# Optimization experiments

Hardware: AMD Instinct MI355X
Metric: run time of the kernel (lower is better)

## Reference

```python
import jax, jax.numpy as jnp
import numpy as np
import math

ALPHA = 2.0   # ATan surrogate default alpha
TAU = 2.0     # LIF tau
VTH = 1.0     # v_threshold default
EPS = 1e-5    # BatchNorm eps
T, N, C, H, W = 16, 32, 128, 32, 32
COUT = 128

@jax.custom_vjp
def atan_spike(x):
    return (x >= 0).astype(x.dtype)

def _spike_fwd(x):
    return (x >= 0).astype(x.dtype), x

def _spike_bwd(x, g):
    return (g * (ALPHA / 2) / (1.0 + (math.pi / 2 * ALPHA * x) ** 2),)

atan_spike.defvjp(_spike_fwd, _spike_bwd)

def lif_scan(x):
    # MultiStepLIFNode, decay_input=False, v_reset=0.0, detach_reset=True:
    #   v <- v + (x_t - (v - 0)) / tau ; spike = H(v - vth) ; v <- v * (1 - sg(spike))
    def step(v, x_t):
        v = v + (x_t - v) / TAU
        s = atan_spike(v - VTH)
        v = v * (1.0 - jax.lax.stop_gradient(s))
        return v, s
    v0 = jnp.zeros_like(x[0])
    _, spikes = jax.lax.scan(step, v0, x)
    return spikes  # [T, N, C, H, W]

def setup_inputs() -> dict:
    key = jax.random.key(0)
    ks = jax.random.split(key, 9)
    x = jax.random.normal(ks[0], (T, N, C, H, W), dtype=jnp.float32)
    dw_w = jax.random.normal(ks[1], (C, 1, 3, 3), dtype=jnp.float32) * (1.0 / 3.0)
    dw_b = jax.random.normal(ks[2], (C,), dtype=jnp.float32) * 0.01
    pw_w = jax.random.normal(ks[3], (COUT, C), dtype=jnp.float32) * (1.0 / math.sqrt(C))
    pw_b = jax.random.normal(ks[4], (COUT,), dtype=jnp.float32) * 0.01
    gamma = jnp.ones((COUT,), dtype=jnp.float32)
    beta = jnp.zeros((COUT,), dtype=jnp.float32)
    run_mean = jax.random.normal(ks[5], (COUT,), dtype=jnp.float32) * 0.1
    run_var = jax.random.uniform(ks[6], (COUT,), dtype=jnp.float32) + 0.5
    return {"x": x, "dw_w": dw_w, "dw_b": dw_b, "pw_w": pw_w, "pw_b": pw_b,
            "gamma": gamma, "beta": beta, "run_mean": run_mean, "run_var": run_var}

def reference(x, dw_w, dw_b, pw_w, pw_b, gamma, beta, run_mean, run_var):
    s = lif_scan(x)                          # [T,N,C,H,W] spikes
    s2 = s.reshape(T * N, C, H, W)           # seq_to_ann_forward flattening
    # depthwise 3x3, stride 1, pad 1
    y = jax.lax.conv_general_dilated(
        s2, dw_w, window_strides=(1, 1), padding="SAME",
        feature_group_count=C,
        dimension_numbers=("NCHW", "OIHW", "NCHW"))
    y = y + dw_b[None, :, None, None]
    # pointwise 1x1
    y = jnp.einsum("nchw,oc->nohw", y, pw_w) + pw_b[None, :, None, None]
    # BatchNorm2d (inference mode, running stats)
    scale = gamma / jnp.sqrt(run_var + EPS)
    y = (y - run_mean[None, :, None, None]) * scale[None, :, None, None] + beta[None, :, None, None]
    return y.reshape(T, N, COUT, H, W)
```

## Files before the change

### kernel.cpp

```cpp
#include <hip/hip_runtime.h>
#include <hip/hip_bf16.h>
#include <stdint.h>

#define T_    16
#define N_    32
#define C_    128
#define HW_   1024
#define COUT_ 128

typedef __bf16 bf16x8 __attribute__((ext_vector_type(8)));
typedef float  f32x4  __attribute__((ext_vector_type(4)));

__global__ __launch_bounds__(256) void k0_prep(
    const float* __restrict__ pw_w, const float* __restrict__ pw_b,
    const float* __restrict__ gamma, const float* __restrict__ beta,
    const float* __restrict__ mean,  const float* __restrict__ var,
    __bf16* __restrict__ wbf, float* __restrict__ scale2, float* __restrict__ bias2) {
  int idx = blockIdx.x * 256 + threadIdx.x;
  if (idx < COUT_ * C_) wbf[idx] = (__bf16)pw_w[idx];
  if (idx < COUT_) {
    float s = gamma[idx] * rsqrtf(var[idx] + 1e-5f);
    scale2[idx] = s;
    bias2[idx]  = beta[idx] + (pw_b[idx] - mean[idx]) * s;
  }
}

__global__ __launch_bounds__(256) void k1_lif(const float* __restrict__ x,
                                              uint32_t* __restrict__ S) {
  int nc   = blockIdx.x;
  int tid  = threadIdx.x;
  int lane = tid & 63;
  int w    = tid >> 6;
  size_t base = (size_t)nc * HW_;
  unsigned long long* S64 = (unsigned long long*)S;

  float v0 = 0.f, v1 = 0.f, v2 = 0.f, v3 = 0.f;
#pragma unroll
  for (int t = 0; t < T_; ++t) {
    const float* xp = x + (size_t)t * (N_ * C_ * HW_) + base;
    float x0 = xp[tid];
    float x1 = xp[256 + tid];
    float x2 = xp[512 + tid];
    float x3 = xp[768 + tid];
    v0 = v0 + (x0 - v0) * 0.5f; bool s0 = (v0 >= 1.0f); if (s0) v0 = 0.f;
    v1 = v1 + (x1 - v1) * 0.5f; bool s1 = (v1 >= 1.0f); if (s1) v1 = 0.f;
    v2 = v2 + (x2 - v2) * 0.5f; bool s2 = (v2 >= 1.0f); if (s2) v2 = 0.f;
    v3 = v3 + (x3 - v3) * 0.5f; bool s3 = (v3 >= 1.0f); if (s3) v3 = 0.f;
    unsigned long long m0 = __ballot(s0);
    unsigned long long m1 = __ballot(s1);
    unsigned long long m2 = __ballot(s2);
    unsigned long long m3 = __ballot(s3);
    if (lane == 0) {
      size_t b64 = ((size_t)nc * T_ + t) * 16;
      S64[b64 + 0  + w] = m0;
      S64[b64 + 4  + w] = m1;
      S64[b64 + 8  + w] = m2;
      S64[b64 + 12 + w] = m3;
    }
  }
}

__global__ __launch_bounds__(256) void k2_main(
    const uint32_t* __restrict__ S,
    const float* __restrict__ dww, const float* __restrict__ dwb,
    const __bf16* __restrict__ wbf,
    const float* __restrict__ scale2, const float* __restrict__ bias2,
    float* __restrict__ out) {
  __shared__ uint32_t sb[C_ * 8];
  __shared__ __bf16  Blds[128 * 136];

  const int bid   = blockIdx.x;
  const int n_img = bid >> 3;
  const int rg    = bid & 7;
  const int t_img = n_img >> 5;
  const int n_in  = n_img & 31;
  const int r0    = rg * 4;
  const int tid   = threadIdx.x;

#pragma unroll
  for (int k = 0; k < 3; ++k) {
    int li = k * 256 + tid;
    int c  = li / 6;
    int ri = li - c * 6;
    int gr = r0 - 1 + ri;
    uint32_t wv = 0;
    if (gr >= 0 && gr < 32)
      wv = S[(((size_t)n_in * C_ + c) * T_ + t_img) * 32 + gr];
    sb[c * 8 + ri] = wv;
  }
  __syncthreads();

  {
    int c    = tid & 127;
    int half = tid >> 7;
    float w9[9];
#pragma unroll
    for (int i = 0; i < 9; ++i) w9[i] = dww[c * 9 + i];
    float bias = dwb[c];
    uint64_t R[6];
#pragma unroll
    for (int q = 0; q < 6; ++q) R[q] = ((uint64_t)sb[c * 8 + q]) << 1;

    int col0 = half * 16;
#pragma unroll 4
    for (int ci = 0; ci < 16; ++ci) {
      int col = col0 + ci;
      float acc[4] = {bias, bias, bias, bias};
#pragma unroll
      for (int q = 0; q < 6; ++q) {
        uint32_t tri = (uint32_t)(R[q] >> col) & 7u;
        float b0 = (float)(tri & 1u);
        float b1 = (float)((tri >> 1) & 1u);
        float b2 = (float)(tri >> 2);
#pragma unroll
        for (int kh = 0; kh < 3; ++kh) {
          int r = q - kh;
          if (r >= 0 && r < 4) {
            acc[r] += w9[kh * 3 + 0] * b0;
            acc[r] += w9[kh * 3 + 1] * b1;
            acc[r] += w9[kh * 3 + 2] * b2;
          }
        }
      }
#pragma unroll
      for (int r = 0; r < 4; ++r)
        Blds[(r * 32 + col) * 136 + c] = (__bf16)acc[r];
    }
  }
  __syncthreads();

  const int lane  = tid & 63;
  const int wid   = tid >> 6;
  const int ohalf = wid >> 1;
  const int hhalf = wid & 1;
  const int m16   = lane & 15;
  const int q4    = lane >> 4;

  f32x4 acc[4][4];
#pragma unroll
  for (int mt = 0; mt < 4; ++mt)
#pragma unroll
    for (int nt = 0; nt < 4; ++nt)
      acc[mt][nt] = (f32x4){0.f, 0.f, 0.f, 0.f};

#pragma unroll
  for (int ks = 0; ks < 4; ++ks) {
    const int k0 = ks * 32 + q4 * 8;
    bf16x8 af[4], bfr[4];
#pragma unroll
    for (int mt = 0; mt < 4; ++mt) {
      int m = ohalf * 64 + mt * 16 + m16;
      af[mt] = *(const bf16x8*)(wbf + m * 128 + k0);
    }
#pragma unroll
    for (int nt = 0; nt < 4; ++nt) {
      int hw = hhalf * 64 + nt * 16 + m16;
      bfr[nt] = *(const bf16x8*)(Blds + hw * 136 + k0);
    }
#pragma unroll
    for (int nt = 0; nt < 4; ++nt)
#pragma unroll
      for (int mt = 0; mt < 4; ++mt)
        acc[mt][nt] = __builtin_amdgcn_mfma_f32_16x16x32_bf16(af[mt], bfr[nt], acc[mt][nt], 0, 0, 0);
  }

#pragma unroll
  for (int mt = 0; mt < 4; ++mt) {
    int ob = ohalf * 64 + mt * 16 + q4 * 4;
    f32x4 sc = *(const f32x4*)(scale2 + ob);
    f32x4 bs = *(const f32x4*)(bias2 + ob);
#pragma unroll
    for (int nt = 0; nt < 4; ++nt) {
      int hw = hhalf * 64 + nt * 16 + m16;
      size_t obase = (size_t)n_img * (COUT_ * HW_) + (size_t)rg * 128 + hw;
#pragma unroll
      for (int ri = 0; ri < 4; ++ri) {
        out[obase + (size_t)(ob + ri) * HW_] = acc[mt][nt][ri] * sc[ri] + bs[ri];
      }
    }
  }
}

extern "C" void kernel_launch(void* const* d_in, const int* in_sizes, int n_in_args,
                              void* d_out, int out_size, void* d_ws, size_t ws_size,
                              hipStream_t stream) {
  const float* x     = (const float*)d_in[0];
  const float* dw_w  = (const float*)d_in[1];
  const float* dw_b  = (const float*)d_in[2];
  const float* pw_w  = (const float*)d_in[3];
  const float* pw_b  = (const float*)d_in[4];
  const float* gamma = (const float*)d_in[5];
  const float* beta  = (const float*)d_in[6];
  const float* rmean = (const float*)d_in[7];
  const float* rvar  = (const float*)d_in[8];
  float* out = (float*)d_out;

  uint32_t* S    = (uint32_t*)d_ws;
  __bf16* wbf    = (__bf16*)((char*)d_ws + (size_t)N_ * C_ * T_ * 128);
  float* scale2  = (float*)((char*)wbf + (size_t)COUT_ * C_ * 2);
  float* bias2   = scale2 + COUT_;

  k0_prep<<<64, 256, 0, stream>>>(pw_w, pw_b, gamma, beta, rmean, rvar, wbf, scale2, bias2);
  k1_lif<<<N_ * C_, 256, 0, stream>>>(x, S);
  k2_main<<<(T_ * N_) * 8, 256, 0, stream>>>(S, dw_w, dw_b, wbf, scale2, bias2, out);
}
```

Before: 495.0 us.

## Vectorize LIF loads with bit interleaving and stage output through LDS

The LIF kernel now loads 4 contiguous floats per thread as one vector and prefetches the next timestep. It interleaves the four ballot masks with a bit-spread so the spike bitmap keeps its original pixel order while 8 lanes write 32-bit words. The main kernel stages the BN-scaled GEMM output in shared memory, in two halves of 64 output channels, and then writes full rows with 128-bit coalesced stores instead of scattered scalar stores. This adds extra LDS traffic and barriers in exchange for better global memory access efficiency.

```diff
diff --git a/kernel.cpp b/kernel.cpp
--- a/kernel.cpp
+++ b/kernel.cpp
@@ -25,38 +25,44 @@
   }
 }
 
+__device__ __forceinline__ uint32_t spread4(uint32_t x) {
+  x = (x | (x << 12)) & 0x000F000Fu;
+  x = (x | (x << 6))  & 0x03030303u;
+  x = (x | (x << 3))  & 0x11111111u;
+  return x;
+}
+
 __global__ __launch_bounds__(256) void k1_lif(const float* __restrict__ x,
                                               uint32_t* __restrict__ S) {
-  int nc   = blockIdx.x;
-  int tid  = threadIdx.x;
-  int lane = tid & 63;
-  int w    = tid >> 6;
-  size_t base = (size_t)nc * HW_;
-  unsigned long long* S64 = (unsigned long long*)S;
-
+  const int nc   = blockIdx.x;
+  const int tid  = threadIdx.x;
+  const int lane = tid & 63;
+  const int w    = tid >> 6;
+  const size_t img = (size_t)N_ * C_ * HW_;
+  const float* xb = x + (size_t)nc * HW_ + (size_t)tid * 4;
+  const int r8 = (lane & 7) * 8;
+
+  f32x4 xv = *(const f32x4*)xb;
   float v0 = 0.f, v1 = 0.f, v2 = 0.f, v3 = 0.f;
 #pragma unroll
   for (int t = 0; t < T_; ++t) {
-    const float* xp = x + (size_t)t * (N_ * C_ * HW_) + base;
-    float x0 = xp[tid];
-    float x1 = xp[256 + tid];
-    float x2 = xp[512 + tid];
-    float x3 = xp[768 + tid];
-    v0 = v0 + (x0 - v0) * 0.5f; bool s0 = (v0 >= 1.0f); if (s0) v0 = 0.f;
-    v1 = v1 + (x1 - v1) * 0.5f; bool s1 = (v1 >= 1.0f); if (s1) v1 = 0.f;
-    v2 = v2 + (x2 - v2) * 0.5f; bool s2 = (v2 >= 1.0f); if (s2) v2 = 0.f;
-    v3 = v3 + (x3 - v3) * 0.5f; bool s3 = (v3 >= 1.0f); if (s3) v3 = 0.f;
-    unsigned long long m0 = __ballot(s0);
-    unsigned long long m1 = __ballot(s1);
-    unsigned long long m2 = __ballot(s2);
-    unsigned long long m3 = __ballot(s3);
-    if (lane == 0) {
-      size_t b64 = ((size_t)nc * T_ + t) * 16;
-      S64[b64 + 0  + w] = m0;
-      S64[b64 + 4  + w] = m1;
-      S64[b64 + 8  + w] = m2;
-      S64[b64 + 12 + w] = m3;
-    }
+    f32x4 cx = xv;
+    if (t < T_ - 1) xv = *(const f32x4*)(xb + img * (size_t)(t + 1));
+    v0 = v0 + (cx[0] - v0) * 0.5f; bool s0 = (v0 >= 1.0f); if (s0) v0 = 0.f;
+    v1 = v1 + (cx[1] - v1) * 0.5f; bool s1 = (v1 >= 1.0f); if (s1) v1 = 0.f;
+    v2 = v2 + (cx[2] - v2) * 0.5f; bool s2 = (v2 >= 1.0f); if (s2) v2 = 0.f;
+    v3 = v3 + (cx[3] - v3) * 0.5f; bool s3 = (v3 >= 1.0f); if (s3) v3 = 0.f;
+    uint64_t m0 = __ballot(s0);
+    uint64_t m1 = __ballot(s1);
+    uint64_t m2 = __ballot(s2);
+    uint64_t m3 = __ballot(s3);
+    uint32_t b0 = (uint32_t)(m0 >> r8) & 0xffu;
+    uint32_t b1 = (uint32_t)(m1 >> r8) & 0xffu;
+    uint32_t b2 = (uint32_t)(m2 >> r8) & 0xffu;
+    uint32_t b3 = (uint32_t)(m3 >> r8) & 0xffu;
+    uint32_t word = spread4(b0) | (spread4(b1) << 1) | (spread4(b2) << 2) | (spread4(b3) << 3);
+    if (lane < 8)
+      S[((size_t)nc * T_ + t) * 32 + w * 8 + lane] = word;
   }
 }
 
@@ -66,8 +72,10 @@
     const __bf16* __restrict__ wbf,
     const float* __restrict__ scale2, const float* __restrict__ bias2,
     float* __restrict__ out) {
-  __shared__ uint32_t sb[C_ * 8];
-  __shared__ __bf16  Blds[128 * 136];
+  __shared__ __align__(16) char smem[4096 + 128 * 136 * 2];
+  uint32_t* sb  = (uint32_t*)smem;
+  __bf16*  Blds = (__bf16*)(smem + 4096);
+  float*   F    = (float*)smem;
 
   const int bid   = blockIdx.x;
   const int n_img = bid >> 3;
@@ -105,7 +113,7 @@
 #pragma unroll 4
     for (int ci = 0; ci < 16; ++ci) {
       int col = col0 + ci;
-      float acc[4] = {bias, bias, bias, bias};
+      float acc4[4] = {bias, bias, bias, bias};
 #pragma unroll
       for (int q = 0; q < 6; ++q) {
         uint32_t tri = (uint32_t)(R[q] >> col) & 7u;
@@ -116,15 +124,15 @@
         for (int kh = 0; kh < 3; ++kh) {
           int r = q - kh;
           if (r >= 0 && r < 4) {
-            acc[r] += w9[kh * 3 + 0] * b0;
-            acc[r] += w9[kh * 3 + 1] * b1;
-            acc[r] += w9[kh * 3 + 2] * b2;
+            acc4[r] += w9[kh * 3 + 0] * b0;
+            acc4[r] += w9[kh * 3 + 1] * b1;
+            acc4[r] += w9[kh * 3 + 2] * b2;
           }
         }
       }
 #pragma unroll
       for (int r = 0; r < 4; ++r)
-        Blds[(r * 32 + col) * 136 + c] = (__bf16)acc[r];
+        Blds[(r * 32 + col) * 136 + c] = (__bf16)acc4[r];
     }
   }
   __syncthreads();
@@ -164,20 +172,37 @@
         acc[mt][nt] = __builtin_amdgcn_mfma_f32_16x16x32_bf16(af[mt], bfr[nt], acc[mt][nt], 0, 0, 0);
   }
 
-#pragma unroll
-  for (int mt = 0; mt < 4; ++mt) {
-    int ob = ohalf * 64 + mt * 16 + q4 * 4;
-    f32x4 sc = *(const f32x4*)(scale2 + ob);
-    f32x4 bs = *(const f32x4*)(bias2 + ob);
-#pragma unroll
-    for (int nt = 0; nt < 4; ++nt) {
-      int hw = hhalf * 64 + nt * 16 + m16;
-      size_t obase = (size_t)n_img * (COUT_ * HW_) + (size_t)rg * 128 + hw;
-#pragma unroll
-      for (int ri = 0; ri < 4; ++ri) {
-        out[obase + (size_t)(ob + ri) * HW_] = acc[mt][nt][ri] * sc[ri] + bs[ri];
+  __syncthreads();
+
+  const size_t outbase = (size_t)n_img * (COUT_ * HW_) + (size_t)rg * 128;
+  const int rrow = tid >> 5;
+  const int cw   = (tid & 31) * 4;
+#pragma unroll
+  for (int g = 0; g < 2; ++g) {
+    if (ohalf == g) {
+#pragma unroll
+      for (int mt = 0; mt < 4; ++mt) {
+        int orow = mt * 16 + q4 * 4;
+        int ob   = g * 64 + orow;
+        f32x4 sc = *(const f32x4*)(scale2 + ob);
+        f32x4 bs = *(const f32x4*)(bias2 + ob);
+#pragma unroll
+        for (int nt = 0; nt < 4; ++nt) {
+          int hw = hhalf * 64 + nt * 16 + m16;
+#pragma unroll
+          for (int ri = 0; ri < 4; ++ri)
+            F[(orow + ri) * 132 + hw] = acc[mt][nt][ri] * sc[ri] + bs[ri];
+        }
       }
     }
+    __syncthreads();
+#pragma unroll
+    for (int i = 0; i < 8; ++i) {
+      int orow = i * 8 + rrow;
+      f32x4 val = *(const f32x4*)(F + orow * 132 + cw);
+      *(f32x4*)(out + outbase + (size_t)(g * 64 + orow) * HW_ + cw) = val;
+    }
+    if (g == 0) __syncthreads();
   }
 }
 
```

After: 508.6 us. 1.03x slower.
